# Performance work log

Measured on AMD Instinct MI355X. Metric: run time of the kernel, lower is better.

Reference implementation:

```python
import jax, jax.numpy as jnp
import numpy as np

B, T, D, H, C, WIN = 2, 2048, 512, 8, 64, 128
EPS = 1e-6


def _rms_norm(x, w):
    # x: (..., C)
    norm = jax.lax.rsqrt(jnp.mean(x * x, axis=-1, keepdims=True) + EPS)
    return x * norm * w


def _apply_rope(x, cos_p, sin_p):
    # x: (B, H, T, C); cos_p/sin_p: (T, C)
    half = x.shape[-1] // 2
    x1, x2 = x[..., :half], x[..., half:]
    rotated = jnp.concatenate([-x2, x1], axis=-1)
    return x * cos_p + rotated * sin_p


def setup_inputs() -> dict:
    key = jax.random.key(0)
    ks = jax.random.split(key, 5)
    h = jax.random.normal(ks[0], (B, T, D), dtype=jnp.float32)
    # RoPE cache (rotate-half convention): (T_max, head_dim)
    inv_freq = 1.0 / (10000.0 ** (jnp.arange(0, C, 2, dtype=jnp.float32) / C))  # (C/2,)
    pos = jnp.arange(T, dtype=jnp.float32)
    freqs = pos[:, None] * inv_freq[None, :]                      # (T, C/2)
    emb = jnp.concatenate([freqs, freqs], axis=-1)                # (T, C)
    rope_cos = jnp.cos(emb)
    rope_sin = jnp.sin(emb)
    scale = 0.02
    W_q = jax.random.normal(ks[1], (D, H * C), dtype=jnp.float32) * scale
    W_k = jax.random.normal(ks[2], (D, H * C), dtype=jnp.float32) * scale
    W_v = jax.random.normal(ks[3], (D, H * C), dtype=jnp.float32) * scale
    W_o = jax.random.normal(ks[4], (H * C, D), dtype=jnp.float32) * scale
    q_norm_w = jnp.ones((C,), dtype=jnp.float32)
    k_norm_w = jnp.ones((C,), dtype=jnp.float32)
    return {"h": h, "rope_cos": rope_cos, "rope_sin": rope_sin,
            "W_q": W_q, "W_k": W_k, "W_v": W_v, "W_o": W_o,
            "q_norm_w": q_norm_w, "k_norm_w": k_norm_w}


def reference(h, rope_cos, rope_sin, W_q, W_k, W_v, W_o, q_norm_w, k_norm_w):
    Bx, Tx, _ = h.shape
    q = (h @ W_q).reshape(Bx, Tx, H, C)
    k = (h @ W_k).reshape(Bx, Tx, H, C)
    v = (h @ W_v).reshape(Bx, Tx, H, C)
    q = _rms_norm(q, q_norm_w)
    k = _rms_norm(k, k_norm_w)
    positions = jnp.arange(Tx)
    cos_p = rope_cos[positions]   # (T, C)
    sin_p = rope_sin[positions]
    # transpose to (B, H, T, C), apply rope, transpose back handled implicitly
    q = _apply_rope(q.transpose(0, 2, 1, 3), cos_p, sin_p).transpose(0, 2, 1, 3)
    k = _apply_rope(k.transpose(0, 2, 1, 3), cos_p, sin_p).transpose(0, 2, 1, 3)
    i = positions[:, None]
    j = positions[None, :]
    sw_mask = (j <= i) & (j > i - WIN)                # (T, T) banded causal
    logits = jnp.einsum('bthc,bshc->bhts', q, k) / np.sqrt(C).astype(np.float32)
    logits = jnp.where(sw_mask[None, None], logits, jnp.float32(-jnp.inf))
    attn = jax.nn.softmax(logits, axis=-1)
    out = jnp.einsum('bhts,bshc->bthc', attn, v).reshape(Bx, Tx, H * C)
    return out @ W_o
```

## Files before the change

kernel.cpp:

```cpp
#include <hip/hip_runtime.h>
#include <hip/hip_bf16.h>
#include <cmath>

#define Tt 2048
#define Hh 8

using u16x8 = __attribute__((ext_vector_type(8))) unsigned short;
using s16x8 = __attribute__((ext_vector_type(8))) short;
using f32x4 = __attribute__((ext_vector_type(4))) float;

__device__ __forceinline__ unsigned short f2bf(float f) {
  __hip_bfloat16 b = __float2bfloat16(f);
  return *reinterpret_cast<unsigned short*>(&b);
}

#define GLD16(gp, lp)                                                        \
  __builtin_amdgcn_global_load_lds(                                          \
      (const __attribute__((address_space(1))) unsigned int*)(gp),           \
      (__attribute__((address_space(3))) unsigned int*)(lp), 16, 0, 0)

__global__ __launch_bounds__(256) void prep_all(
    const float* __restrict__ s0, const float* __restrict__ s1,
    const float* __restrict__ s2, const float* __restrict__ s3,
    unsigned short* __restrict__ d,
    const float* __restrict__ hsrc, unsigned short* __restrict__ hdst) {
  int tid = threadIdx.x;
  if (blockIdx.z == 4) {
    int gid = ((int)blockIdx.y * 8 + blockIdx.x) * 256 + tid;
    #pragma unroll
    for (int s = 0; s < 16; ++s) {
      size_t i = ((size_t)s * 16384 + gid) * 8;
      const float4* g = (const float4*)&hsrc[i];
      float4 f0 = g[0], f1 = g[1];
      u16x8 o = {f2bf(f0.x), f2bf(f0.y), f2bf(f0.z), f2bf(f0.w),
                 f2bf(f1.x), f2bf(f1.y), f2bf(f1.z), f2bf(f1.w)};
      *(u16x8*)&hdst[i] = o;
    }
    return;
  }
  __shared__ unsigned short tile[64 * 65];
  const float* srcs[4] = {s0, s1, s2, s3};
  const float* src = srcs[blockIdx.z];
  unsigned short* dst = d + (size_t)blockIdx.z * 512 * 512;
  int n0 = blockIdx.x * 64, k0 = blockIdx.y * 64;
  int tx = tid & 63, ty = tid >> 6;
  #pragma unroll
  for (int i = 0; i < 16; ++i) {
    int k = ty * 16 + i;
    tile[k * 65 + tx] = f2bf(src[(k0 + k) * 512 + n0 + tx]);
  }
  __syncthreads();
  #pragma unroll
  for (int i = 0; i < 16; ++i) {
    int n = ty * 16 + i;
    dst[(n0 + n) * 512 + k0 + tx] = tile[tx * 65 + n];
  }
}

__global__ __launch_bounds__(256) void qkv_fused(
    const unsigned short* __restrict__ Hb,
    const unsigned short* __restrict__ WTall,
    const float* __restrict__ qnw, const float* __restrict__ knw,
    const float* __restrict__ rcos, const float* __restrict__ rsin,
    unsigned short* __restrict__ Qw, unsigned short* __restrict__ Kw,
    unsigned short* __restrict__ Vw) {
  __shared__ alignas(16) unsigned short S[24576];
  int tid = threadIdx.x;
  int wave = tid >> 6, lane = tid & 63;
  int ln = lane & 15, qd = lane >> 4;
  int m0 = blockIdx.x * 128;
  int gh = blockIdx.y;
  int n0 = gh * 64;

  f32x4 acc[2][4];
  #pragma unroll
  for (int mi = 0; mi < 2; ++mi)
    #pragma unroll
    for (int ni = 0; ni < 4; ++ni) acc[mi][ni] = f32x4{0.f, 0.f, 0.f, 0.f};

  auto stage = [&](int k0, int buf) {
    char* Apt = (char*)(S + buf * 12288);
    char* Bpt = (char*)(S + buf * 12288 + 8192);
    #pragma unroll
    for (int s = 0; s < 4; ++s) {
      int q = s * 4 + wave;
      int L = q * 64 + lane;
      int row = L >> 3;
      int cb = (L & 7) ^ (row & 7);
      GLD16(&Hb[(size_t)(m0 + row) * 512 + k0 + cb * 8], Apt + q * 1024);
    }
    #pragma unroll
    for (int s = 0; s < 2; ++s) {
      int q = s * 4 + wave;
      int L = q * 64 + lane;
      int row = L >> 3;
      int cb = (L & 7) ^ (row & 7);
      GLD16(&WTall[(size_t)(n0 + row) * 512 + k0 + cb * 8], Bpt + q * 1024);
    }
  };

  stage(0, 0);
  __syncthreads();
  for (int it = 0; it < 8; ++it) {
    int cur = it & 1;
    if (it < 7) stage((it + 1) * 64, cur ^ 1);
    const char* Al = (const char*)(S + cur * 12288);
    const char* Bl = (const char*)(S + cur * 12288 + 8192);
    #pragma unroll
    for (int half = 0; half < 2; ++half) {
      s16x8 af[2], bfr[4];
      #pragma unroll
      for (int mi = 0; mi < 2; ++mi) {
        int ar = wave * 32 + mi * 16 + ln;
        int cbp = (qd + half * 4) ^ (ar & 7);
        af[mi] = *(const s16x8*)(Al + ar * 128 + cbp * 16);
      }
      #pragma unroll
      for (int ni = 0; ni < 4; ++ni) {
        int br = ni * 16 + ln;
        int cbp = (qd + half * 4) ^ (br & 7);
        bfr[ni] = *(const s16x8*)(Bl + br * 128 + cbp * 16);
      }
      #pragma unroll
      for (int mi = 0; mi < 2; ++mi)
        #pragma unroll
        for (int ni = 0; ni < 4; ++ni)
          acc[mi][ni] = __builtin_amdgcn_mfma_f32_16x16x32_bf16(
              af[mi], bfr[ni], acc[mi][ni], 0, 0, 0);
    }
    __syncthreads();
  }

  int mat = gh >> 3, head = gh & 7;
  const float* nw = (mat == 0) ? qnw : knw;
  bool do_rope = (mat < 2);
  int mrow0 = m0 + wave * 32;
  int b = mrow0 >> 11, tb = mrow0 & (Tt - 1);

  #pragma unroll
  for (int mi = 0; mi < 2; ++mi) {
    float vals[4][4];
    #pragma unroll
    for (int ni = 0; ni < 4; ++ni)
      #pragma unroll
      for (int r = 0; r < 4; ++r) vals[ni][r] = acc[mi][ni][r];

    if (do_rope) {
      #pragma unroll
      for (int r = 0; r < 4; ++r) {
        float ss = 0.f;
        #pragma unroll
        for (int ni = 0; ni < 4; ++ni) ss += vals[ni][r] * vals[ni][r];
        ss += __shfl_xor(ss, 1, 64);
        ss += __shfl_xor(ss, 2, 64);
        ss += __shfl_xor(ss, 4, 64);
        ss += __shfl_xor(ss, 8, 64);
        float nrm = rsqrtf(ss * (1.0f / 64.0f) + 1e-6f);
        #pragma unroll
        for (int ni = 0; ni < 4; ++ni) vals[ni][r] *= nrm;
      }
      #pragma unroll
      for (int ni = 0; ni < 4; ++ni) {
        float w = nw[ni * 16 + ln];
        #pragma unroll
        for (int r = 0; r < 4; ++r) vals[ni][r] *= w;
      }
      float res[4][4];
      #pragma unroll
      for (int r = 0; r < 4; ++r) {
        int t = tb + mi * 16 + qd * 4 + r;
        #pragma unroll
        for (int ni = 0; ni < 4; ++ni) {
          int c = ni * 16 + ln;
          float cs = rcos[t * 64 + c];
          float sn = rsin[t * 64 + c];
          float part = vals[ni ^ 2][r];
          float rot = (ni < 2) ? -part : part;
          res[ni][r] = vals[ni][r] * cs + rot * sn;
        }
      }
      #pragma unroll
      for (int ni = 0; ni < 4; ++ni)
        #pragma unroll
        for (int r = 0; r < 4; ++r) vals[ni][r] = res[ni][r];
    }

    if (mat < 2) {
      unsigned short* Wl = S + wave * 2304;
      #pragma unroll
      for (int ni = 0; ni < 4; ++ni)
        #pragma unroll
        for (int r = 0; r < 4; ++r)
          Wl[(mi * 16 + qd * 4 + r) * 72 + ni * 16 + ln] = f2bf(vals[ni][r]);
    } else {
      unsigned short* Wl = S + wave * 2560;
      #pragma unroll
      for (int ni = 0; ni < 4; ++ni)
        #pragma unroll
        for (int r = 0; r < 4; ++r)
          Wl[(ni * 16 + ln) * 40 + mi * 16 + qd * 4 + r] = f2bf(vals[ni][r]);
    }
  }

  if (mat < 2) {
    unsigned short* Wl = S + wave * 2304;
    unsigned short* Og =
        ((mat == 0) ? Qw : Kw) + (((size_t)b * Hh + head) * Tt + tb) * 64;
    #pragma unroll
    for (int i = 0; i < 4; ++i) {
      int idx = i * 64 + lane;
      int rr = idx >> 3, cc = (idx & 7) * 8;
      *(u16x8*)&Og[rr * 64 + cc] = *(const u16x8*)&Wl[rr * 72 + cc];
    }
  } else {
    unsigned short* Wl = S + wave * 2560;
    unsigned short* Og = Vw + ((size_t)b * Hh + head) * 64 * 2048 + tb;
    #pragma unroll
    for (int i = 0; i < 4; ++i) {
      int idx = i * 64 + lane;
      int rr = idx >> 2, cc = (idx & 3) * 8;
      *(u16x8*)&Og[(size_t)rr * 2048 + cc] = *(const u16x8*)&Wl[rr * 40 + cc];
    }
  }
}

__global__ __launch_bounds__(256) void attn_mfma(
    const unsigned short* __restrict__ Q,
    const unsigned short* __restrict__ K,
    const unsigned short* __restrict__ Vg,
    unsigned short* __restrict__ AO) {
  __shared__ alignas(16) unsigned short KP[192 * 72];
  __shared__ alignas(16) unsigned short Vt[64 * 200];
  int tid = threadIdx.x;
  int wave = tid >> 6, lane = tid & 63;
  int ln = lane & 15, qd = lane >> 4;
  int t0 = blockIdx.x * 64, bh = blockIdx.y;
  int kb = t0 - 128;
  int q0 = wave * 16;

  const unsigned short* Kg = K + (size_t)bh * Tt * 64;
  const unsigned short* Vb = Vg + (size_t)bh * 64 * 2048;

  int srow = tid >> 2, scol = (tid & 3) * 16;
  #pragma unroll
  for (int p = 0; p < 3; ++p) {
    int row = p * 64 + srow;
    int kg = kb + row; if (kg < 0) kg = 0;
    const u16x8* gk = (const u16x8*)&Kg[(size_t)kg * 64 + scol];
    u16x8 k0v = gk[0], k1v = gk[1];
    *(u16x8*)&KP[row * 72 + scol] = k0v;
    *(u16x8*)&KP[row * 72 + scol + 8] = k1v;
  }
  #pragma unroll
  for (int j = 0; j < 3; ++j)
    #pragma unroll
    for (int it = 0; it < 2; ++it) {
      int idx = it * 256 + tid;
      int row = idx >> 3, ch = (idx & 7) * 8;
      u16x8 v = *(const u16x8*)&Vb[(size_t)row * 2048 + kb + j * 64 + ch];
      *(u16x8*)&Vt[row * 200 + j * 64 + ch] = v;
    }
  const unsigned short* Qg = Q + ((size_t)bh * Tt + t0 + q0) * 64;
  s16x8 aq0 = *(const s16x8*)&Qg[ln * 64 + qd * 8];
  s16x8 aq1 = *(const s16x8*)&Qg[ln * 64 + 32 + qd * 8];
  __syncthreads();

  f32x4 sf[12];
  #pragma unroll
  for (int nt = 0; nt < 12; ++nt) {
    s16x8 b0 = *(const s16x8*)&KP[(nt * 16 + ln) * 72 + qd * 8];
    s16x8 b1 = *(const s16x8*)&KP[(nt * 16 + ln) * 72 + 32 + qd * 8];
    f32x4 a = {0.f, 0.f, 0.f, 0.f};
    a = __builtin_amdgcn_mfma_f32_16x16x32_bf16(aq0, b0, a, 0, 0, 0);
    a = __builtin_amdgcn_mfma_f32_16x16x32_bf16(aq1, b1, a, 0, 0, 0);
    sf[nt] = a;
  }
  __syncthreads();

  unsigned short* Pl = KP;
  int ok0 = (t0 < 128) ? (128 - t0) : 0;
  #pragma unroll
  for (int r = 0; r < 4; ++r) {
    int lq = q0 + qd * 4 + r;
    float mx = -INFINITY;
    #pragma unroll
    for (int nt = 0; nt < 12; ++nt) {
      int kk = nt * 16 + ln;
      bool valid = (kk > lq) && (kk <= lq + 128) && (kk >= ok0);
      float s = valid ? sf[nt][r] * 0.125f : -INFINITY;
      sf[nt][r] = s;
      mx = fmaxf(mx, s);
    }
    mx = fmaxf(mx, __shfl_xor(mx, 1, 64));
    mx = fmaxf(mx, __shfl_xor(mx, 2, 64));
    mx = fmaxf(mx, __shfl_xor(mx, 4, 64));
    mx = fmaxf(mx, __shfl_xor(mx, 8, 64));
    float sum = 0.f;
    #pragma unroll
    for (int nt = 0; nt < 12; ++nt) {
      float e = __expf(sf[nt][r] - mx);
      sf[nt][r] = e;
      sum += e;
    }
    sum += __shfl_xor(sum, 1, 64);
    sum += __shfl_xor(sum, 2, 64);
    sum += __shfl_xor(sum, 4, 64);
    sum += __shfl_xor(sum, 8, 64);
    float inv = 1.0f / sum;
    #pragma unroll
    for (int nt = 0; nt < 12; ++nt)
      Pl[lq * 200 + nt * 16 + ln] = f2bf(sf[nt][r] * inv);
  }

  f32x4 oa[4] = {f32x4{0,0,0,0}, f32x4{0,0,0,0}, f32x4{0,0,0,0}, f32x4{0,0,0,0}};
  #pragma unroll
  for (int s = 0; s < 6; ++s) {
    s16x8 ap = *(const s16x8*)&Pl[(q0 + ln) * 200 + s * 32 + qd * 8];
    #pragma unroll
    for (int nt = 0; nt < 4; ++nt) {
      s16x8 bv = *(const s16x8*)&Vt[(nt * 16 + ln) * 200 + s * 32 + qd * 8];
      oa[nt] = __builtin_amdgcn_mfma_f32_16x16x32_bf16(ap, bv, oa[nt], 0, 0, 0);
    }
  }

  unsigned short* Ow = KP + q0 * 200;
  #pragma unroll
  for (int ni = 0; ni < 4; ++ni)
    #pragma unroll
    for (int r = 0; r < 4; ++r)
      Ow[(qd * 4 + r) * 72 + ni * 16 + ln] = f2bf(oa[ni][r]);
  int b = bh >> 3, h = bh & 7;
  #pragma unroll
  for (int i = 0; i < 2; ++i) {
    int idx = i * 64 + lane;
    int rr = idx >> 3, cc = (idx & 7) * 8;
    *(u16x8*)&AO[((size_t)(b * Tt + t0 + q0 + rr) * Hh + h) * 64 + cc] =
        *(const u16x8*)&Ow[rr * 72 + cc];
  }
}

__global__ __launch_bounds__(256) void out_gemm(
    const unsigned short* __restrict__ Am,
    const unsigned short* __restrict__ WT,
    float* __restrict__ Out) {
  __shared__ alignas(16) unsigned short S[16384];
  int tid = threadIdx.x;
  int wave = tid >> 6, lane = tid & 63;
  int ln = lane & 15, qd = lane >> 4;
  int wm = wave >> 1, wn = wave & 1;
  int m0 = blockIdx.x * 64, n0 = blockIdx.y * 64;

  f32x4 acc[2][2];
  #pragma unroll
  for (int mi = 0; mi < 2; ++mi)
    #pragma unroll
    for (int ni = 0; ni < 2; ++ni) acc[mi][ni] = f32x4{0.f, 0.f, 0.f, 0.f};

  auto stage = [&](int k0, int buf) {
    char* Apt = (char*)(S + buf * 8192);
    char* Bpt = (char*)(S + buf * 8192 + 4096);
    #pragma unroll
    for (int s = 0; s < 2; ++s) {
      int q = s * 4 + wave;
      int L = q * 64 + lane;
      int row = L >> 3;
      int cb = (L & 7) ^ (row & 7);
      GLD16(&Am[(size_t)(m0 + row) * 512 + k0 + cb * 8], Apt + q * 1024);
      GLD16(&WT[(size_t)(n0 + row) * 512 + k0 + cb * 8], Bpt + q * 1024);
    }
  };

  stage(0, 0);
  __syncthreads();
  for (int it = 0; it < 8; ++it) {
    int cur = it & 1;
    if (it < 7) stage((it + 1) * 64, cur ^ 1);
    const char* Al = (const char*)(S + cur * 8192);
    const char* Bl = (const char*)(S + cur * 8192 + 4096);
    #pragma unroll
    for (int half = 0; half < 2; ++half) {
      s16x8 af[2], bfr[2];
      #pragma unroll
      for (int mi = 0; mi < 2; ++mi) {
        int ar = wm * 32 + mi * 16 + ln;
        int cbp = (qd + half * 4) ^ (ar & 7);
        af[mi] = *(const s16x8*)(Al + ar * 128 + cbp * 16);
      }
      #pragma unroll
      for (int ni = 0; ni < 2; ++ni) {
        int br = wn * 32 + ni * 16 + ln;
        int cbp = (qd + half * 4) ^ (br & 7);
        bfr[ni] = *(const s16x8*)(Bl + br * 128 + cbp * 16);
      }
      #pragma unroll
      for (int mi = 0; mi < 2; ++mi)
        #pragma unroll
        for (int ni = 0; ni < 2; ++ni)
          acc[mi][ni] = __builtin_amdgcn_mfma_f32_16x16x32_bf16(
              af[mi], bfr[ni], acc[mi][ni], 0, 0, 0);
    }
    __syncthreads();
  }

  #pragma unroll
  for (int mi = 0; mi < 2; ++mi)
    #pragma unroll
    for (int r = 0; r < 4; ++r) {
      int row = m0 + wm * 32 + mi * 16 + qd * 4 + r;
      #pragma unroll
      for (int ni = 0; ni < 2; ++ni)
        Out[(size_t)row * 512 + n0 + wn * 32 + ni * 16 + ln] = acc[mi][ni][r];
    }
}

extern "C" void kernel_launch(void* const* d_in, const int* in_sizes, int n_in,
                              void* d_out, int out_size, void* d_ws,
                              size_t ws_size, hipStream_t stream) {
  const float* h   = (const float*)d_in[0];
  const float* rc  = (const float*)d_in[1];
  const float* rs  = (const float*)d_in[2];
  const float* Wq  = (const float*)d_in[3];
  const float* Wk  = (const float*)d_in[4];
  const float* Wv  = (const float*)d_in[5];
  const float* Wo  = (const float*)d_in[6];
  const float* qnw = (const float*)d_in[7];
  const float* knw = (const float*)d_in[8];

  unsigned short* ws    = (unsigned short*)d_ws;
  unsigned short* WTall = ws;
  unsigned short* WTo   = WTall + 1536 * 512;
  unsigned short* Hb    = WTo + 512 * 512;
  unsigned short* Qw    = Hb + 2097152;
  unsigned short* Kw    = Qw + 2097152;
  unsigned short* Vw    = Kw + 2097152;
  unsigned short* AOw   = Vw + 2097152;

  prep_all<<<dim3(8, 8, 5), 256, 0, stream>>>(Wq, Wk, Wv, Wo, WTall, h, Hb);

  qkv_fused<<<dim3(32, 24), 256, 0, stream>>>(Hb, WTall, qnw, knw, rc, rs,
                                              Qw, Kw, Vw);

  attn_mfma<<<dim3(32, 16), 256, 0, stream>>>(Qw, Kw, Vw, AOw);

  out_gemm<<<dim3(64, 8), 256, 0, stream>>>(AOw, WTo, (float*)d_out);
}
```

Before: 105.9 us.

## Use async LDS loads with XOR swizzle in attention and remap block IDs for locality

The attention kernel now stages K and V tiles with direct global-to-LDS 16-byte loads into unpadded, XOR-swizzled layouts instead of register round-trips into padded arrays. The P and V reads in the second MFMA loop use matching swizzled indices, and s_setprio raises wave priority around the MFMA loops. All three kernels remap the linear block index, which on AMD typically spreads consecutive blocks across XCDs so tiles sharing data land on the same L2. The swizzle logic, including the 24-chunk V row mapping, adds index math and must stay consistent to remain correct.

```diff
diff --git a/kernel.cpp b/kernel.cpp
--- a/kernel.cpp
+++ b/kernel.cpp
@@ -68,8 +68,10 @@
   int tid = threadIdx.x;
   int wave = tid >> 6, lane = tid & 63;
   int ln = lane & 15, qd = lane >> 4;
-  int m0 = blockIdx.x * 128;
-  int gh = blockIdx.y;
+  int id = (int)blockIdx.x + 32 * (int)blockIdx.y;
+  int sw = (id & 7) * 96 + (id >> 3);
+  int m0 = (sw & 31) * 128;
+  int gh = sw >> 5;
   int n0 = gh * 64;
 
   f32x4 acc[2][4];
@@ -229,52 +231,58 @@
     const unsigned short* __restrict__ K,
     const unsigned short* __restrict__ Vg,
     unsigned short* __restrict__ AO) {
-  __shared__ alignas(16) unsigned short KP[192 * 72];
-  __shared__ alignas(16) unsigned short Vt[64 * 200];
+  __shared__ alignas(16) unsigned short KP[192 * 64];
+  __shared__ alignas(16) unsigned short Vt[64 * 192];
   int tid = threadIdx.x;
   int wave = tid >> 6, lane = tid & 63;
   int ln = lane & 15, qd = lane >> 4;
-  int t0 = blockIdx.x * 64, bh = blockIdx.y;
+  int id = (int)blockIdx.x + 32 * (int)blockIdx.y;
+  int swb = (id & 7) * 64 + (id >> 3);
+  int t0 = (swb & 31) * 64, bh = swb >> 5;
   int kb = t0 - 128;
   int q0 = wave * 16;
 
   const unsigned short* Kg = K + (size_t)bh * Tt * 64;
   const unsigned short* Vb = Vg + (size_t)bh * 64 * 2048;
 
-  int srow = tid >> 2, scol = (tid & 3) * 16;
-  #pragma unroll
-  for (int p = 0; p < 3; ++p) {
-    int row = p * 64 + srow;
+  #pragma unroll
+  for (int s = 0; s < 6; ++s) {
+    int q = s * 4 + wave;
+    int L = q * 64 + lane;
+    int row = L >> 3;
     int kg = kb + row; if (kg < 0) kg = 0;
-    const u16x8* gk = (const u16x8*)&Kg[(size_t)kg * 64 + scol];
-    u16x8 k0v = gk[0], k1v = gk[1];
-    *(u16x8*)&KP[row * 72 + scol] = k0v;
-    *(u16x8*)&KP[row * 72 + scol + 8] = k1v;
-  }
-  #pragma unroll
-  for (int j = 0; j < 3; ++j)
-    #pragma unroll
-    for (int it = 0; it < 2; ++it) {
-      int idx = it * 256 + tid;
-      int row = idx >> 3, ch = (idx & 7) * 8;
-      u16x8 v = *(const u16x8*)&Vb[(size_t)row * 2048 + kb + j * 64 + ch];
-      *(u16x8*)&Vt[row * 200 + j * 64 + ch] = v;
-    }
+    int cb = (L & 7) ^ (row & 7);
+    GLD16(&Kg[(size_t)kg * 64 + cb * 8], (char*)KP + q * 1024);
+  }
+  #pragma unroll
+  for (int s = 0; s < 6; ++s) {
+    int q = s * 4 + wave;
+    int L = q * 64 + lane;
+    int row = L / 24;
+    int c24 = L - row * 24;
+    int cb = (c24 & ~7) | ((c24 & 7) ^ (row & 7));
+    GLD16(&Vb[(size_t)row * 2048 + kb + cb * 8], (char*)Vt + q * 1024);
+  }
   const unsigned short* Qg = Q + ((size_t)bh * Tt + t0 + q0) * 64;
   s16x8 aq0 = *(const s16x8*)&Qg[ln * 64 + qd * 8];
   s16x8 aq1 = *(const s16x8*)&Qg[ln * 64 + 32 + qd * 8];
   __syncthreads();
 
+  int swk0 = ((qd) ^ (ln & 7)) * 8;
+  int swk1 = ((qd + 4) ^ (ln & 7)) * 8;
   f32x4 sf[12];
+  __builtin_amdgcn_s_setprio(1);
   #pragma unroll
   for (int nt = 0; nt < 12; ++nt) {
-    s16x8 b0 = *(const s16x8*)&KP[(nt * 16 + ln) * 72 + qd * 8];
-    s16x8 b1 = *(const s16x8*)&KP[(nt * 16 + ln) * 72 + 32 + qd * 8];
+    const unsigned short* kr = &KP[(nt * 16 + ln) * 64];
+    s16x8 b0 = *(const s16x8*)&kr[swk0];
+    s16x8 b1 = *(const s16x8*)&kr[swk1];
     f32x4 a = {0.f, 0.f, 0.f, 0.f};
     a = __builtin_amdgcn_mfma_f32_16x16x32_bf16(aq0, b0, a, 0, 0, 0);
     a = __builtin_amdgcn_mfma_f32_16x16x32_bf16(aq1, b1, a, 0, 0, 0);
     sf[nt] = a;
   }
+  __builtin_amdgcn_s_setprio(0);
   __syncthreads();
 
   unsigned short* Pl = KP;
@@ -308,22 +316,30 @@
     sum += __shfl_xor(sum, 8, 64);
     float inv = 1.0f / sum;
     #pragma unroll
-    for (int nt = 0; nt < 12; ++nt)
-      Pl[lq * 200 + nt * 16 + ln] = f2bf(sf[nt][r] * inv);
+    for (int nt = 0; nt < 12; ++nt) {
+      int kk = nt * 16 + ln;
+      int c = kk >> 3;
+      int swc = (c & ~7) | ((c & 7) ^ (lq & 7));
+      Pl[lq * 192 + swc * 8 + (kk & 7)] = f2bf(sf[nt][r] * inv);
+    }
   }
 
   f32x4 oa[4] = {f32x4{0,0,0,0}, f32x4{0,0,0,0}, f32x4{0,0,0,0}, f32x4{0,0,0,0}};
+  __builtin_amdgcn_s_setprio(1);
   #pragma unroll
   for (int s = 0; s < 6; ++s) {
-    s16x8 ap = *(const s16x8*)&Pl[(q0 + ln) * 200 + s * 32 + qd * 8];
+    int c = s * 4 + qd;
+    int swc = (c & ~7) | ((c & 7) ^ (ln & 7));
+    s16x8 ap = *(const s16x8*)&Pl[(q0 + ln) * 192 + swc * 8];
     #pragma unroll
     for (int nt = 0; nt < 4; ++nt) {
-      s16x8 bv = *(const s16x8*)&Vt[(nt * 16 + ln) * 200 + s * 32 + qd * 8];
+      s16x8 bv = *(const s16x8*)&Vt[(nt * 16 + ln) * 192 + swc * 8];
       oa[nt] = __builtin_amdgcn_mfma_f32_16x16x32_bf16(ap, bv, oa[nt], 0, 0, 0);
     }
   }
-
-  unsigned short* Ow = KP + q0 * 200;
+  __builtin_amdgcn_s_setprio(0);
+
+  unsigned short* Ow = KP + q0 * 192;
   #pragma unroll
   for (int ni = 0; ni < 4; ++ni)
     #pragma unroll
@@ -348,7 +364,9 @@
   int wave = tid >> 6, lane = tid & 63;
   int ln = lane & 15, qd = lane >> 4;
   int wm = wave >> 1, wn = wave & 1;
-  int m0 = blockIdx.x * 64, n0 = blockIdx.y * 64;
+  int id = (int)blockIdx.x + 64 * (int)blockIdx.y;
+  int swb = (id & 7) * 64 + (id >> 3);
+  int m0 = (swb & 63) * 64, n0 = (swb >> 6) * 64;
 
   f32x4 acc[2][2];
   #pragma unroll
```

Measured after the change: 105.9 us. Within noise of the previous version (-0.0%).
